# Optimization experiments

Measured on AMD Instinct MI355X. Metric: run time of the kernel, lower is better.

## Reference

```python
import jax, jax.numpy as jnp
import numpy as np

N_NODES = 500_000
N_EDGES = 8_000_000
N_GRAPHS = 512
N_FEATURES = 128
HIDDEN = 128
N_FILT = 8
OUT_DIM = 64
BN_EPS = 1e-5


def setup_inputs() -> dict:
    key = jax.random.key(0)
    ks = jax.random.split(key, 16)
    rn = lambda k, shape, s=0.05: jax.random.normal(k, shape, jnp.float32) * s
    return {
        "x": jax.random.normal(ks[0], (N_NODES, N_FEATURES), jnp.float32),
        "W1": rn(ks[1], (N_FEATURES, HIDDEN)),
        "b1": jnp.zeros((HIDDEN,), jnp.float32),
        "W2": rn(ks[2], (HIDDEN, N_FILT)),
        "b2": jnp.zeros((N_FILT,), jnp.float32),
        "W0": rn(ks[3], (2 * N_FILT, OUT_DIM)),
        "b0": jnp.zeros((OUT_DIM,), jnp.float32),
        "g1W": rn(ks[4], (OUT_DIM, OUT_DIM)),
        "g1b": jnp.zeros((OUT_DIM,), jnp.float32),
        "l1W": rn(ks[5], (OUT_DIM, OUT_DIM)),
        "g2W": rn(ks[6], (OUT_DIM, N_FEATURES)),
        "g2b": jnp.zeros((N_FEATURES,), jnp.float32),
        "l2W": rn(ks[7], (OUT_DIM, N_FEATURES)),
        "bn_gamma": jnp.ones((N_FEATURES,), jnp.float32),
        "bn_beta": jnp.zeros((N_FEATURES,), jnp.float32),
        "edge_index": jax.random.randint(ks[8], (2, N_EDGES), 0, N_NODES),
        "batch": jnp.sort(jax.random.randint(ks[9], (N_NODES,), 0, N_GRAPHS)),
        "death_edge_idx": jax.random.randint(ks[10], (N_NODES,), 0, N_EDGES),
    }


def _deepset(x, batch, GW, Gb, LW):
    # scatter-mean over graphs, Linear (no bias), gather-broadcast subtract
    sums = jax.ops.segment_sum(x, batch, num_segments=N_GRAPHS)  # [G, d]
    cnt = jax.ops.segment_sum(jnp.ones((x.shape[0], 1), x.dtype), batch,
                              num_segments=N_GRAPHS)             # [G, 1]
    xm = (sums / jnp.maximum(cnt, 1.0)) @ LW                      # Lambda
    return x @ GW + Gb - xm[batch]                                # Gamma - gather


def reference(x, W1, b1, W2, b2, W0, b0, g1W, g1b, l1W, g2W, g2b, l2W,
              bn_gamma, bn_beta, edge_index, batch, death_edge_idx):
    # filtrations MLP: [N, F] -> [N, n_filtrations]
    filtered_v = jax.nn.relu(x @ W1 + b1) @ W2 + b2
    # edge filtration = max of endpoint values (gather + max), [E, n_filtrations]
    filtered_e = jnp.maximum(filtered_v[edge_index[0]], filtered_v[edge_index[1]])
    # persistence pairs (lower-star 0-dim generators): birth = vertex value,
    # death = paired edge value; layout [N, n_filt, 2] -> [N, 2*n_filt]
    births = filtered_v
    deaths = filtered_e[death_edge_idx]
    x0 = jnp.stack([births, deaths], axis=-1).reshape(x.shape[0], 2 * N_FILT)
    # set_fn: Linear -> ReLU -> DeepSet -> ReLU -> DeepSet
    x0 = jax.nn.relu(x0 @ W0 + b0)
    x0 = jax.nn.relu(_deepset(x0, batch, g1W, g1b, l1W))
    x0 = _deepset(x0, batch, g2W, g2b, l2W)
    # residual: x + BatchNorm1d(relu(x0)) with batch statistics
    h = jax.nn.relu(x0)
    mu = h.mean(axis=0)
    var = h.var(axis=0)
    hn = (h - mu) * jax.lax.rsqrt(var + BN_EPS)
    return x + hn * bn_gamma + bn_beta
```

## Files before the change

kernel.cpp:

```cpp
#include <hip/hip_runtime.h>
#include <hip/hip_bf16.h>

#define NNODES 500000
#define NEDGES 8000000
#define NGRAPHS 512
#define NFEAT 128
#define NHID 128
#define NFILT 8
#define ODIM 64
#define BN_EPS 1e-5f
#define NBLK2 3907
#define NBLK3 7813
#define NBLK4 977

typedef __attribute__((ext_vector_type(8))) short bf16x8;
typedef __attribute__((ext_vector_type(4))) float f32x4;
#define MFMA16(a, b, c) __builtin_amdgcn_mfma_f32_16x16x32_bf16(a, b, c, 0, 0, 0)

__device__ inline ushort f2bs(float f) {
  union { __hip_bfloat16 h; ushort u; } cv;
  cv.h = __float2bfloat16(f);
  return cv.u;
}

__global__ void k_pack(const float* __restrict__ g1W, const float* __restrict__ g2W,
                       const float* __restrict__ W1, const int* __restrict__ batch,
                       ushort* __restrict__ pW1, ushort* __restrict__ pW2,
                       ushort* __restrict__ pW0, int* __restrict__ cnt) {
  int idx = blockIdx.x * 256 + threadIdx.x;
  if (idx < 4096) {
    int j = idx & 7, l = (idx >> 3) & 63, kb = (idx >> 9) & 1, ncb = idx >> 10;
    int k = kb * 32 + (l >> 4) * 8 + j, c = ncb * 16 + (l & 15);
    pW1[idx] = f2bs(g1W[k * 64 + c]);
  }
  if (idx < 8192) {
    int j = idx & 7, l = (idx >> 3) & 63, kb = (idx >> 9) & 1, ncb = idx >> 10;
    int k = kb * 32 + (l >> 4) * 8 + j, c = ncb * 16 + (l & 15);
    pW2[idx] = f2bs(g2W[k * 128 + c]);
  }
  if (idx < 16384) {
    int j = idx & 7, l = (idx >> 3) & 63, kb = (idx >> 9) & 3, ncb = idx >> 11;
    int k = kb * 32 + (l >> 4) * 8 + j, c = ncb * 16 + (l & 15);
    pW0[idx] = f2bs(W1[k * 128 + c]);
  }
  if (idx < NGRAPHS) {
    int g = idx;
    int lo0 = 0, hi0 = NNODES;
    while (lo0 < hi0) { int mid = (lo0 + hi0) >> 1; if (batch[mid] < g) lo0 = mid + 1; else hi0 = mid; }
    int lo1 = lo0, hi1 = NNODES;
    while (lo1 < hi1) { int mid = (lo1 + hi1) >> 1; if (batch[mid] < g + 1) lo1 = mid + 1; else hi1 = mid; }
    cnt[g] = lo1 - lo0;
  }
}

__global__ __launch_bounds__(256) void k_filt(
    const float* __restrict__ x, const ushort* __restrict__ pW0,
    const float* __restrict__ b1, const float* __restrict__ W2,
    const float* __restrict__ b2, float* __restrict__ fv) {
  __shared__ float w2s[128 * 12];
  const int t = threadIdx.x;
  for (int i = t; i < 1024; i += 256) {
    int c = i >> 3, f = i & 7;
    w2s[c * 12 + f] = W2[i];
  }
  __syncthreads();
  const int wv = t >> 6, l = t & 63;
  const int lr = l & 15, lg = l >> 4;
  const int n0 = blockIdx.x * 128 + wv * 32;
  if (n0 >= NNODES) return;

  union { uint4 u; bf16x8 b; } bf[2][4];
#pragma unroll
  for (int mt = 0; mt < 2; ++mt)
#pragma unroll
    for (int kb = 0; kb < 4; ++kb) {
      const float* src = &x[(size_t)(n0 + mt * 16 + lr) * 128 + kb * 32 + lg * 8];
      float v[8];
      *(float4*)&v[0] = *(const float4*)src;
      *(float4*)&v[4] = *(const float4*)(src + 4);
      ushort s[8];
#pragma unroll
      for (int e = 0; e < 8; ++e) s[e] = f2bs(v[e]);
      bf[mt][kb].u = *(uint4*)s;
    }

  float pf0[8], pf1[8];
#pragma unroll
  for (int f = 0; f < 8; ++f) { pf0[f] = 0.f; pf1[f] = 0.f; }

#pragma unroll
  for (int ncb = 0; ncb < 8; ++ncb) {
    union { uint4 u; bf16x8 b; } af[4];
#pragma unroll
    for (int kb = 0; kb < 4; ++kb)
      af[kb].u = *(const uint4*)&pW0[((ncb * 4 + kb) * 64 + l) * 8];
    f32x4 a0 = (f32x4){0.f, 0.f, 0.f, 0.f};
    f32x4 a1 = (f32x4){0.f, 0.f, 0.f, 0.f};
#pragma unroll
    for (int kb = 0; kb < 4; ++kb) {
      a0 = MFMA16(af[kb].b, bf[0][kb].b, a0);
      a1 = MFMA16(af[kb].b, bf[1][kb].b, a1);
    }
    float bbv[4];
    *(float4*)bbv = *(const float4*)&b1[ncb * 16 + lg * 4];
#pragma unroll
    for (int r = 0; r < 4; ++r) {
      const int c = ncb * 16 + lg * 4 + r;
      float h0 = fmaxf(a0[r] + bbv[r], 0.f);
      float h1 = fmaxf(a1[r] + bbv[r], 0.f);
      float w20[4], w21[4];
      *(float4*)w20 = *(const float4*)&w2s[c * 12];
      *(float4*)w21 = *(const float4*)&w2s[c * 12 + 4];
#pragma unroll
      for (int f = 0; f < 4; ++f) {
        pf0[f]     = fmaf(h0, w20[f], pf0[f]);
        pf0[f + 4] = fmaf(h0, w21[f], pf0[f + 4]);
        pf1[f]     = fmaf(h1, w20[f], pf1[f]);
        pf1[f + 4] = fmaf(h1, w21[f], pf1[f + 4]);
      }
    }
  }
#pragma unroll
  for (int f = 0; f < 8; ++f) {
    pf0[f] += __shfl_xor(pf0[f], 16); pf0[f] += __shfl_xor(pf0[f], 32);
    pf1[f] += __shfl_xor(pf1[f], 16); pf1[f] += __shfl_xor(pf1[f], 32);
  }
  if (lg == 0) {
    float o0[8], o1[8];
#pragma unroll
    for (int f = 0; f < 8; ++f) {
      float bb = b2[f];
      o0[f] = pf0[f] + bb;
      o1[f] = pf1[f] + bb;
    }
    *(float4*)&fv[(size_t)(n0 + lr) * 8]          = *(float4*)&o0[0];
    *(float4*)&fv[(size_t)(n0 + lr) * 8 + 4]      = *(float4*)&o0[4];
    *(float4*)&fv[(size_t)(n0 + 16 + lr) * 8]     = *(float4*)&o1[0];
    *(float4*)&fv[(size_t)(n0 + 16 + lr) * 8 + 4] = *(float4*)&o1[4];
  }
}

__global__ __launch_bounds__(256) void k_pairs(
    const float* __restrict__ fv, const int* __restrict__ edge_index,
    const int* __restrict__ didx, const int* __restrict__ batch,
    const float* __restrict__ W0, const float* __restrict__ b0,
    ushort* __restrict__ y, float* __restrict__ sums1) {
  __shared__ float w0s[16 * 64];
  __shared__ float b0s[64];
  __shared__ float ps[4][64];
  __shared__ int pg[4];
  const int t = threadIdx.x;
  for (int i = t; i < 1024; i += 256) w0s[i] = W0[i];
  if (t < 64) b0s[t] = b0[t];
  __syncthreads();

  const int wv = t >> 6, j = t & 63;
  const int n0 = blockIdx.x * 128 + wv * 32;

  int de = 0, gg = -1, uu = 0, vvx = 0;
  if (j < 32) {
    int nn = n0 + j;
    if (nn < NNODES) { de = didx[nn]; gg = batch[nn]; }
  }
  if (j < 32 && gg >= 0) { uu = edge_index[de]; vvx = edge_index[NEDGES + de]; }

  const float bb = b0s[j];
  float acc0 = 0.f, acc1 = 0.f;
  int g_first = -1, g_second = -1;

#pragma unroll 4
  for (int i = 0; i < 32; ++i) {
    int g = __shfl(gg, i);
    if (g >= 0) {
      int u = __shfl(uu, i);
      int v = __shfl(vvx, i);
      int n = n0 + i;
      float nb[8], ub[8], vb[8];
      *(float4*)&nb[0] = *(const float4*)&fv[(size_t)n * 8];
      *(float4*)&nb[4] = *(const float4*)&fv[(size_t)n * 8 + 4];
      *(float4*)&ub[0] = *(const float4*)&fv[(size_t)u * 8];
      *(float4*)&ub[4] = *(const float4*)&fv[(size_t)u * 8 + 4];
      *(float4*)&vb[0] = *(const float4*)&fv[(size_t)v * 8];
      *(float4*)&vb[4] = *(const float4*)&fv[(size_t)v * 8 + 4];
      float a = bb;
#pragma unroll
      for (int f = 0; f < 8; ++f) {
        a = fmaf(nb[f], w0s[(2 * f) * 64 + j], a);
        a = fmaf(fmaxf(ub[f], vb[f]), w0s[(2 * f + 1) * 64 + j], a);
      }
      a = fmaxf(a, 0.f);
      y[(size_t)n * 64 + j] = f2bs(a);
      if (g_first < 0) g_first = g;
      if (g == g_first) acc0 += a;
      else { g_second = g; acc1 += a; }
    }
  }
  if (g_second >= 0) atomicAdd(&sums1[g_second * 64 + j], acc1);
  ps[wv][j] = acc0;
  if (j == 0) pg[wv] = g_first;
  __syncthreads();

  if (t < 64) {
    const int bg = pg[0];
    float s = 0.f;
#pragma unroll
    for (int w = 0; w < 4; ++w) {
      const int gv = pg[w];
      if (gv < 0) continue;
      if (gv == bg) s += ps[w][t];
      else atomicAdd(&sums1[gv * 64 + t], ps[w][t]);
    }
    if (bg >= 0) atomicAdd(&sums1[bg * 64 + t], s);
  }
}

template <int D>
__global__ void k_meanlin(const float* __restrict__ sums,
                          const int* __restrict__ cnt,
                          const float* __restrict__ LW,
                          float* __restrict__ xm) {
  __shared__ float m[64];
  const int g = blockIdx.x, t = threadIdx.x;
  const float c = fmaxf((float)cnt[g], 1.f);
  if (t < 64) m[t] = sums[g * 64 + t] / c;
  __syncthreads();
  float a = 0.f;
#pragma unroll
  for (int k = 0; k < 64; ++k) a = fmaf(m[k], LW[k * D + t], a);
  xm[g * D + t] = a;
}

__global__ __launch_bounds__(256) void k_ds1(
    const ushort* __restrict__ ybf, const int* __restrict__ batch,
    const ushort* __restrict__ pW1, const float* __restrict__ g1b,
    const float* __restrict__ xm1, ushort* __restrict__ y2,
    float* __restrict__ sums2) {
  __shared__ float ps[4][64];
  __shared__ int pg[4];
  const int t = threadIdx.x, wv = t >> 6, l = t & 63;
  const int lr = l & 15, lg = l >> 4, c0 = lg * 4;
  const int nbase = blockIdx.x * 512;

  union { uint4 u; bf16x8 b; } af[4][2];
#pragma unroll
  for (int ncb = 0; ncb < 4; ++ncb)
#pragma unroll
    for (int kb = 0; kb < 2; ++kb)
      af[ncb][kb].u = *(const uint4*)&pW1[((ncb * 2 + kb) * 64 + l) * 8];

  for (int tile = 0; tile < 4; ++tile) {
    const int n0 = nbase + tile * 128 + wv * 32;
    if (n0 < NNODES) {
      union { uint4 u; bf16x8 b; } bf[2][2];
#pragma unroll
      for (int mt = 0; mt < 2; ++mt)
#pragma unroll
        for (int kb = 0; kb < 2; ++kb)
          bf[mt][kb].u = *(const uint4*)&ybf[(size_t)(n0 + mt * 16 + lr) * 64 + kb * 32 + lg * 8];

      f32x4 acc[2][4];
#pragma unroll
      for (int mt = 0; mt < 2; ++mt)
#pragma unroll
        for (int ncb = 0; ncb < 4; ++ncb) {
          acc[mt][ncb] = (f32x4){0.f, 0.f, 0.f, 0.f};
          acc[mt][ncb] = MFMA16(af[ncb][0].b, bf[mt][0].b, acc[mt][ncb]);
          acc[mt][ncb] = MFMA16(af[ncb][1].b, bf[mt][1].b, acc[mt][ncb]);
        }

      const int g0 = batch[n0 + lr], g1 = batch[n0 + 16 + lr];
      const int g_first = __shfl(g0, 0);

      float wsum[4][4];
#pragma unroll
      for (int ncb = 0; ncb < 4; ++ncb)
#pragma unroll
        for (int r = 0; r < 4; ++r) wsum[ncb][r] = 0.f;

#pragma unroll
      for (int mt = 0; mt < 2; ++mt) {
        const int n = n0 + mt * 16 + lr;
        const int g = mt ? g1 : g0;
        const bool prim = (g == g_first);
#pragma unroll
        for (int ncb = 0; ncb < 4; ++ncb) {
          const int c = ncb * 16 + c0;
          float xmv[4], bbv[4];
          *(float4*)xmv = *(const float4*)&xm1[g * 64 + c];
          *(float4*)bbv = *(const float4*)&g1b[c];
          ushort st[4];
#pragma unroll
          for (int r = 0; r < 4; ++r) {
            float v = fmaxf(acc[mt][ncb][r] + bbv[r] - xmv[r], 0.f);
            st[r] = f2bs(v);
            if (prim) wsum[ncb][r] += v;
            else atomicAdd(&sums2[g * 64 + c + r], v);
          }
          *(ushort4*)&y2[(size_t)n * 64 + c] = *(ushort4*)st;
        }
      }
#pragma unroll
      for (int ncb = 0; ncb < 4; ++ncb)
#pragma unroll
        for (int r = 0; r < 4; ++r) {
          float w = wsum[ncb][r];
          w += __shfl_xor(w, 1); w += __shfl_xor(w, 2);
          w += __shfl_xor(w, 4); w += __shfl_xor(w, 8);
          if (lr == 0) ps[wv][ncb * 16 + c0 + r] = w;
        }
      if (l == 0) pg[wv] = g_first;
    } else {
      ps[wv][l] = 0.f;
      if (l == 0) pg[wv] = -1;
    }
    __syncthreads();

    if (t < 64) {
      const int bg = pg[0];
      float s = 0.f;
#pragma unroll
      for (int w = 0; w < 4; ++w) {
        const int gv = pg[w];
        if (gv < 0) continue;
        if (gv == bg) s += ps[w][t];
        else atomicAdd(&sums2[gv * 64 + t], ps[w][t]);
      }
      if (bg >= 0) atomicAdd(&sums2[bg * 64 + t], s);
    }
    __syncthreads();
  }
}

__global__ __launch_bounds__(256) void k_ds2a(
    const ushort* __restrict__ y2, const int* __restrict__ batch,
    const ushort* __restrict__ pW2, const float* __restrict__ g2b,
    const float* __restrict__ xm2,
    float* __restrict__ pmu, float* __restrict__ psq) {
  __shared__ float ps[4][128], pq[4][128];
  const int t = threadIdx.x, wv = t >> 6, l = t & 63;
  const int lr = l & 15, lg = l >> 4, c0 = lg * 4;
  const int nbase = blockIdx.x * 512;

  float sw[8][4], sq[8][4];
#pragma unroll
  for (int ncb = 0; ncb < 8; ++ncb)
#pragma unroll
    for (int r = 0; r < 4; ++r) { sw[ncb][r] = 0.f; sq[ncb][r] = 0.f; }

  for (int tile = 0; tile < 4; ++tile) {
    const int n0 = nbase + tile * 128 + wv * 32;
    if (n0 >= NNODES) continue;

    union { uint4 u; bf16x8 b; } bf[2][2];
#pragma unroll
    for (int mt = 0; mt < 2; ++mt)
#pragma unroll
      for (int kb = 0; kb < 2; ++kb)
        bf[mt][kb].u = *(const uint4*)&y2[(size_t)(n0 + mt * 16 + lr) * 64 + kb * 32 + lg * 8];

    const int g0 = batch[n0 + lr], g1 = batch[n0 + 16 + lr];

#pragma unroll
    for (int ncb = 0; ncb < 8; ++ncb) {
      union { uint4 u; bf16x8 b; } af0, af1;
      af0.u = *(const uint4*)&pW2[((ncb * 2 + 0) * 64 + l) * 8];
      af1.u = *(const uint4*)&pW2[((ncb * 2 + 1) * 64 + l) * 8];
      f32x4 a0 = (f32x4){0.f, 0.f, 0.f, 0.f}, a1 = (f32x4){0.f, 0.f, 0.f, 0.f};
      a0 = MFMA16(af0.b, bf[0][0].b, a0); a0 = MFMA16(af1.b, bf[0][1].b, a0);
      a1 = MFMA16(af0.b, bf[1][0].b, a1); a1 = MFMA16(af1.b, bf[1][1].b, a1);

      const int c = ncb * 16 + c0;
      float xm0[4], xm1v[4], bbv[4];
      *(float4*)xm0 = *(const float4*)&xm2[g0 * 128 + c];
      *(float4*)xm1v = *(const float4*)&xm2[g1 * 128 + c];
      *(float4*)bbv = *(const float4*)&g2b[c];
#pragma unroll
      for (int r = 0; r < 4; ++r) {
        float v0 = fmaxf(a0[r] + bbv[r] - xm0[r], 0.f);
        float v1 = fmaxf(a1[r] + bbv[r] - xm1v[r], 0.f);
        sw[ncb][r] += v0 + v1;
        sq[ncb][r] = fmaf(v0, v0, fmaf(v1, v1, sq[ncb][r]));
      }
    }
  }

#pragma unroll
  for (int ncb = 0; ncb < 8; ++ncb)
#pragma unroll
    for (int r = 0; r < 4; ++r) {
      float wr = sw[ncb][r], qr = sq[ncb][r];
      wr += __shfl_xor(wr, 1); wr += __shfl_xor(wr, 2);
      wr += __shfl_xor(wr, 4); wr += __shfl_xor(wr, 8);
      qr += __shfl_xor(qr, 1); qr += __shfl_xor(qr, 2);
      qr += __shfl_xor(qr, 4); qr += __shfl_xor(qr, 8);
      if (lr == 0) { ps[wv][ncb * 16 + c0 + r] = wr; pq[wv][ncb * 16 + c0 + r] = qr; }
    }
  __syncthreads();
  if (t < 128) {
    pmu[(size_t)blockIdx.x * 128 + t] = ps[0][t] + ps[1][t] + ps[2][t] + ps[3][t];
    psq[(size_t)blockIdx.x * 128 + t] = pq[0][t] + pq[1][t] + pq[2][t] + pq[3][t];
  }
}

__global__ void k_red(const float* __restrict__ pmu, const float* __restrict__ psq,
                      float* __restrict__ musum, float* __restrict__ sqsum) {
  const int f = threadIdx.x & 127;
  const bool mu = threadIdx.x < 128;
  const float* src = mu ? pmu : psq;
  float s = 0.f;
  for (int b = blockIdx.x; b < NBLK4; b += 32) s += src[(size_t)b * 128 + f];
  atomicAdd(mu ? &musum[f] : &sqsum[f], s);
}

__global__ __launch_bounds__(256) void k_bn(
    const ushort* __restrict__ y2, const int* __restrict__ batch,
    const ushort* __restrict__ pW2, const float* __restrict__ g2b,
    const float* __restrict__ xm2, const float* __restrict__ x,
    const float* __restrict__ musum, const float* __restrict__ sqsum,
    const float* __restrict__ gamma, const float* __restrict__ beta,
    float* __restrict__ out) {
  __shared__ float vs[64 * 132];
  __shared__ float smu[128], ssc[128], sbe[128];
  const int t = threadIdx.x, wv = t >> 6, l = t & 63;
  const int lr = l & 15, lg = l >> 4, c0 = lg * 4;
  if (t < 128) {
    const float invN = 1.f / (float)NNODES;
    float m = musum[t] * invN;
    float v = sqsum[t] * invN - m * m;
    smu[t] = m;
    ssc[t] = rsqrtf(v + BN_EPS) * gamma[t];
    sbe[t] = beta[t];
  }
  const int nblk = blockIdx.x * 64;
  const int n0 = nblk + wv * 16;

  if (n0 < NNODES) {
    union { uint4 u; bf16x8 b; } bf[2];
#pragma unroll
    for (int kb = 0; kb < 2; ++kb)
      bf[kb].u = *(const uint4*)&y2[(size_t)(n0 + lr) * 64 + kb * 32 + lg * 8];

    const int g0 = batch[n0 + lr];
    const int row0 = wv * 16 + lr;

#pragma unroll
    for (int ncb = 0; ncb < 8; ++ncb) {
      union { uint4 u; bf16x8 b; } af0, af1;
      af0.u = *(const uint4*)&pW2[((ncb * 2 + 0) * 64 + l) * 8];
      af1.u = *(const uint4*)&pW2[((ncb * 2 + 1) * 64 + l) * 8];
      f32x4 a0 = (f32x4){0.f, 0.f, 0.f, 0.f};
      a0 = MFMA16(af0.b, bf[0].b, a0);
      a0 = MFMA16(af1.b, bf[1].b, a0);

      const int c = ncb * 16 + c0;
      float bbv[4], xm0[4], hvv[4];
      *(float4*)bbv = *(const float4*)&g2b[c];
      *(float4*)xm0 = *(const float4*)&xm2[g0 * 128 + c];
#pragma unroll
      for (int r = 0; r < 4; ++r)
        hvv[r] = fmaxf(a0[r] + bbv[r] - xm0[r], 0.f);
      *(float4*)&vs[row0 * 132 + c] = *(float4*)hvv;
    }
  }
  __syncthreads();

  const int rmax = NNODES - nblk;
  for (int i = t; i < 2048; i += 256) {
    const int row = i >> 5, c4 = (i & 31) * 4;
    if (row >= rmax) break;
    const int n = nblk + row;
    float hv[4], muv[4], scv[4], bev[4], xv[4], o[4];
    *(float4*)hv = *(const float4*)&vs[row * 132 + c4];
    *(float4*)muv = *(const float4*)&smu[c4];
    *(float4*)scv = *(const float4*)&ssc[c4];
    *(float4*)bev = *(const float4*)&sbe[c4];
    *(float4*)xv = *(const float4*)&x[(size_t)n * 128 + c4];
#pragma unroll
    for (int r = 0; r < 4; ++r)
      o[r] = xv[r] + (hv[r] - muv[r]) * scv[r] + bev[r];
    *(float4*)&out[(size_t)n * 128 + c4] = *(float4*)o;
  }
}

extern "C" void kernel_launch(void* const* d_in, const int* in_sizes, int n_in,
                              void* d_out, int out_size, void* d_ws,
                              size_t ws_size, hipStream_t stream) {
  const float* x     = (const float*)d_in[0];
  const float* W1    = (const float*)d_in[1];
  const float* b1    = (const float*)d_in[2];
  const float* W2    = (const float*)d_in[3];
  const float* b2    = (const float*)d_in[4];
  const float* W0    = (const float*)d_in[5];
  const float* b0    = (const float*)d_in[6];
  const float* g1W   = (const float*)d_in[7];
  const float* g1b   = (const float*)d_in[8];
  const float* l1W   = (const float*)d_in[9];
  const float* g2W   = (const float*)d_in[10];
  const float* g2b   = (const float*)d_in[11];
  const float* l2W   = (const float*)d_in[12];
  const float* gamma = (const float*)d_in[13];
  const float* beta  = (const float*)d_in[14];
  const int* edge_index = (const int*)d_in[15];
  const int* batch      = (const int*)d_in[16];
  const int* didx       = (const int*)d_in[17];
  float* out = (float*)d_out;

  char* ws = (char*)d_ws;
  float*  fv    = (float*) (ws + 0);
  float*  pmu   = (float*) (ws + 0);
  float*  psq   = (float*) (ws + 2000384);
  ushort* ybf   = (ushort*)(ws + 16000000);
  ushort* y2    = (ushort*)(ws + 80000000);
  float*  sums1 = (float*) (ws + 144000000);
  float*  sums2 = (float*) (ws + 144131072);
  float*  musum = (float*) (ws + 144262144);
  float*  sqsum = (float*) (ws + 144262656);
  int*    cnt   = (int*)   (ws + 144263168);
  float*  xm1   = (float*) (ws + 144265216);
  float*  xm2   = (float*) (ws + 144396288);
  ushort* pW1   = (ushort*)(ws + 144658432);
  ushort* pW2   = (ushort*)(ws + 144666624);
  ushort* pW0   = (ushort*)(ws + 144683008);

  hipMemsetAsync(ws + 144000000, 0, 263168, stream);

  k_pack<<<64, 256, 0, stream>>>(g1W, g2W, W1, batch, pW1, pW2, pW0, cnt);
  k_filt<<<NBLK2, 256, 0, stream>>>(x, pW0, b1, W2, b2, fv);
  k_pairs<<<NBLK2, 256, 0, stream>>>(fv, edge_index, didx, batch, W0, b0, ybf, sums1);
  k_meanlin<64><<<NGRAPHS, 64, 0, stream>>>(sums1, cnt, l1W, xm1);
  k_ds1<<<NBLK4, 256, 0, stream>>>(ybf, batch, pW1, g1b, xm1, y2, sums2);
  k_meanlin<128><<<NGRAPHS, 128, 0, stream>>>(sums2, cnt, l2W, xm2);
  k_ds2a<<<NBLK4, 256, 0, stream>>>(y2, batch, pW2, g2b, xm2, pmu, psq);
  k_red<<<32, 256, 0, stream>>>(pmu, psq, musum, sqsum);
  k_bn<<<NBLK3, 256, 0, stream>>>(y2, batch, pW2, g2b, xm2, x, musum, sqsum,
                                  gamma, beta, out);
}
```

Measured before the change: 541.3 us.

## Store filtration values as bf16 and compute pair linear layer with MFMA

Filtration values are now written as bf16, which halves the fv buffer and the bytes moved by the random gathers in the pairs kernel. The 16x64 pair linear layer moves from per-lane scalar FMAs to a bf16 MFMA, using a zero-padded packed W0 built in the pack kernel. Each pairs block now covers four 128-node tiles, and per-graph sums are reduced with shuffles before the atomics. In exchange, births and deaths lose precision to bf16, and nodes outside the first graph of a wave fall back to per-element atomics.

```diff
diff --git a/kernel.cpp b/kernel.cpp
--- a/kernel.cpp
+++ b/kernel.cpp
@@ -24,9 +24,11 @@
 }
 
 __global__ void k_pack(const float* __restrict__ g1W, const float* __restrict__ g2W,
-                       const float* __restrict__ W1, const int* __restrict__ batch,
+                       const float* __restrict__ W1, const float* __restrict__ W0,
+                       const int* __restrict__ batch,
                        ushort* __restrict__ pW1, ushort* __restrict__ pW2,
-                       ushort* __restrict__ pW0, int* __restrict__ cnt) {
+                       ushort* __restrict__ pW0, ushort* __restrict__ pW0p,
+                       int* __restrict__ cnt) {
   int idx = blockIdx.x * 256 + threadIdx.x;
   if (idx < 4096) {
     int j = idx & 7, l = (idx >> 3) & 63, kb = (idx >> 9) & 1, ncb = idx >> 10;
@@ -42,6 +44,11 @@
     int j = idx & 7, l = (idx >> 3) & 63, kb = (idx >> 9) & 3, ncb = idx >> 11;
     int k = kb * 32 + (l >> 4) * 8 + j, c = ncb * 16 + (l & 15);
     pW0[idx] = f2bs(W1[k * 128 + c]);
+  }
+  if (idx < 4096) {
+    int j = idx & 7, l = (idx >> 3) & 63, ncb = idx >> 9;
+    int k = (l >> 4) * 8 + j, c = ncb * 16 + (l & 15);
+    pW0p[idx] = (k < 16) ? f2bs(W0[k * 64 + c]) : (ushort)0;
   }
   if (idx < NGRAPHS) {
     int g = idx;
@@ -56,7 +63,7 @@
 __global__ __launch_bounds__(256) void k_filt(
     const float* __restrict__ x, const ushort* __restrict__ pW0,
     const float* __restrict__ b1, const float* __restrict__ W2,
-    const float* __restrict__ b2, float* __restrict__ fv) {
+    const float* __restrict__ b2, ushort* __restrict__ fv16) {
   __shared__ float w2s[128 * 12];
   const int t = threadIdx.x;
   for (int i = t; i < 1024; i += 256) {
@@ -126,91 +133,132 @@
     pf1[f] += __shfl_xor(pf1[f], 16); pf1[f] += __shfl_xor(pf1[f], 32);
   }
   if (lg == 0) {
-    float o0[8], o1[8];
+    ushort s0[8], s1[8];
 #pragma unroll
     for (int f = 0; f < 8; ++f) {
       float bb = b2[f];
-      o0[f] = pf0[f] + bb;
-      o1[f] = pf1[f] + bb;
-    }
-    *(float4*)&fv[(size_t)(n0 + lr) * 8]          = *(float4*)&o0[0];
-    *(float4*)&fv[(size_t)(n0 + lr) * 8 + 4]      = *(float4*)&o0[4];
-    *(float4*)&fv[(size_t)(n0 + 16 + lr) * 8]     = *(float4*)&o1[0];
-    *(float4*)&fv[(size_t)(n0 + 16 + lr) * 8 + 4] = *(float4*)&o1[4];
+      s0[f] = f2bs(pf0[f] + bb);
+      s1[f] = f2bs(pf1[f] + bb);
+    }
+    *(uint4*)&fv16[(size_t)(n0 + lr) * 8]      = *(uint4*)s0;
+    *(uint4*)&fv16[(size_t)(n0 + 16 + lr) * 8] = *(uint4*)s1;
   }
 }
 
 __global__ __launch_bounds__(256) void k_pairs(
-    const float* __restrict__ fv, const int* __restrict__ edge_index,
+    const ushort* __restrict__ fv16, const int* __restrict__ edge_index,
     const int* __restrict__ didx, const int* __restrict__ batch,
-    const float* __restrict__ W0, const float* __restrict__ b0,
+    const ushort* __restrict__ pW0p, const float* __restrict__ b0,
     ushort* __restrict__ y, float* __restrict__ sums1) {
-  __shared__ float w0s[16 * 64];
-  __shared__ float b0s[64];
   __shared__ float ps[4][64];
   __shared__ int pg[4];
-  const int t = threadIdx.x;
-  for (int i = t; i < 1024; i += 256) w0s[i] = W0[i];
-  if (t < 64) b0s[t] = b0[t];
-  __syncthreads();
-
-  const int wv = t >> 6, j = t & 63;
-  const int n0 = blockIdx.x * 128 + wv * 32;
-
-  int de = 0, gg = -1, uu = 0, vvx = 0;
-  if (j < 32) {
-    int nn = n0 + j;
-    if (nn < NNODES) { de = didx[nn]; gg = batch[nn]; }
-  }
-  if (j < 32 && gg >= 0) { uu = edge_index[de]; vvx = edge_index[NEDGES + de]; }
-
-  const float bb = b0s[j];
-  float acc0 = 0.f, acc1 = 0.f;
-  int g_first = -1, g_second = -1;
-
-#pragma unroll 4
-  for (int i = 0; i < 32; ++i) {
-    int g = __shfl(gg, i);
-    if (g >= 0) {
-      int u = __shfl(uu, i);
-      int v = __shfl(vvx, i);
-      int n = n0 + i;
-      float nb[8], ub[8], vb[8];
-      *(float4*)&nb[0] = *(const float4*)&fv[(size_t)n * 8];
-      *(float4*)&nb[4] = *(const float4*)&fv[(size_t)n * 8 + 4];
-      *(float4*)&ub[0] = *(const float4*)&fv[(size_t)u * 8];
-      *(float4*)&ub[4] = *(const float4*)&fv[(size_t)u * 8 + 4];
-      *(float4*)&vb[0] = *(const float4*)&fv[(size_t)v * 8];
-      *(float4*)&vb[4] = *(const float4*)&fv[(size_t)v * 8 + 4];
-      float a = bb;
-#pragma unroll
-      for (int f = 0; f < 8; ++f) {
-        a = fmaf(nb[f], w0s[(2 * f) * 64 + j], a);
-        a = fmaf(fmaxf(ub[f], vb[f]), w0s[(2 * f + 1) * 64 + j], a);
-      }
-      a = fmaxf(a, 0.f);
-      y[(size_t)n * 64 + j] = f2bs(a);
-      if (g_first < 0) g_first = g;
-      if (g == g_first) acc0 += a;
-      else { g_second = g; acc1 += a; }
-    }
-  }
-  if (g_second >= 0) atomicAdd(&sums1[g_second * 64 + j], acc1);
-  ps[wv][j] = acc0;
-  if (j == 0) pg[wv] = g_first;
-  __syncthreads();
-
-  if (t < 64) {
-    const int bg = pg[0];
-    float s = 0.f;
-#pragma unroll
-    for (int w = 0; w < 4; ++w) {
-      const int gv = pg[w];
-      if (gv < 0) continue;
-      if (gv == bg) s += ps[w][t];
-      else atomicAdd(&sums1[gv * 64 + t], ps[w][t]);
-    }
-    if (bg >= 0) atomicAdd(&sums1[bg * 64 + t], s);
+  const int t = threadIdx.x, wv = t >> 6, l = t & 63;
+  const int lr = l & 15, lg = l >> 4, c0 = lg * 4;
+  const int nbase = blockIdx.x * 512;
+
+  union { uint4 u; bf16x8 b; } af[4];
+#pragma unroll
+  for (int ncb = 0; ncb < 4; ++ncb)
+    af[ncb].u = *(const uint4*)&pW0p[(ncb * 64 + l) * 8];
+
+  for (int tile = 0; tile < 4; ++tile) {
+    const int n0 = nbase + tile * 128 + wv * 32;
+    if (n0 < NNODES) {
+      union { uint4 u; bf16x8 b; } bf[2];
+      int gN[2];
+#pragma unroll
+      for (int mt = 0; mt < 2; ++mt) {
+        const int n = n0 + mt * 16 + lr;
+        gN[mt] = batch[n];
+        bf[mt].u = make_uint4(0u, 0u, 0u, 0u);
+        if (lg < 2) {
+          const int de = didx[n];
+          const int u = edge_index[de];
+          const int v = edge_index[NEDGES + de];
+          ushort4 bb = *(const ushort4*)&fv16[(size_t)n * 8 + lg * 4];
+          ushort4 ub = *(const ushort4*)&fv16[(size_t)u * 8 + lg * 4];
+          ushort4 vb = *(const ushort4*)&fv16[(size_t)v * 8 + lg * 4];
+          const ushort* bp = (const ushort*)&bb;
+          const ushort* up = (const ushort*)&ub;
+          const ushort* vp = (const ushort*)&vb;
+          ushort s[8];
+#pragma unroll
+          for (int j = 0; j < 4; ++j) {
+            s[2 * j] = bp[j];
+            float uf = __uint_as_float((unsigned)up[j] << 16);
+            float vf = __uint_as_float((unsigned)vp[j] << 16);
+            s[2 * j + 1] = (uf > vf) ? up[j] : vp[j];
+          }
+          bf[mt].u = *(uint4*)s;
+        }
+      }
+
+      f32x4 acc[2][4];
+#pragma unroll
+      for (int mt = 0; mt < 2; ++mt)
+#pragma unroll
+        for (int ncb = 0; ncb < 4; ++ncb) {
+          acc[mt][ncb] = (f32x4){0.f, 0.f, 0.f, 0.f};
+          acc[mt][ncb] = MFMA16(af[ncb].b, bf[mt].b, acc[mt][ncb]);
+        }
+
+      const int g_first = __shfl(gN[0], 0);
+      float wsum[4][4];
+#pragma unroll
+      for (int ncb = 0; ncb < 4; ++ncb)
+#pragma unroll
+        for (int r = 0; r < 4; ++r) wsum[ncb][r] = 0.f;
+
+#pragma unroll
+      for (int mt = 0; mt < 2; ++mt) {
+        const int n = n0 + mt * 16 + lr;
+        const int g = gN[mt];
+        const bool prim = (g == g_first);
+#pragma unroll
+        for (int ncb = 0; ncb < 4; ++ncb) {
+          const int c = ncb * 16 + c0;
+          float bbv[4];
+          *(float4*)bbv = *(const float4*)&b0[c];
+          ushort st[4];
+#pragma unroll
+          for (int r = 0; r < 4; ++r) {
+            float v = fmaxf(acc[mt][ncb][r] + bbv[r], 0.f);
+            st[r] = f2bs(v);
+            if (prim) wsum[ncb][r] += v;
+            else atomicAdd(&sums1[g * 64 + c + r], v);
+          }
+          *(ushort4*)&y[(size_t)n * 64 + c] = *(ushort4*)st;
+        }
+      }
+#pragma unroll
+      for (int ncb = 0; ncb < 4; ++ncb)
+#pragma unroll
+        for (int r = 0; r < 4; ++r) {
+          float w = wsum[ncb][r];
+          w += __shfl_xor(w, 1); w += __shfl_xor(w, 2);
+          w += __shfl_xor(w, 4); w += __shfl_xor(w, 8);
+          if (lr == 0) ps[wv][ncb * 16 + c0 + r] = w;
+        }
+      if (l == 0) pg[wv] = g_first;
+    } else {
+      ps[wv][l] = 0.f;
+      if (l == 0) pg[wv] = -1;
+    }
+    __syncthreads();
+
+    if (t < 64) {
+      const int bg = pg[0];
+      float s = 0.f;
+#pragma unroll
+      for (int w = 0; w < 4; ++w) {
+        const int gv = pg[w];
+        if (gv < 0) continue;
+        if (gv == bg) s += ps[w][t];
+        else atomicAdd(&sums1[gv * 64 + t], ps[w][t]);
+      }
+      if (bg >= 0) atomicAdd(&sums1[bg * 64 + t], s);
+    }
+    __syncthreads();
   }
 }
 
@@ -506,7 +554,7 @@
   float* out = (float*)d_out;
 
   char* ws = (char*)d_ws;
-  float*  fv    = (float*) (ws + 0);
+  ushort* fv16  = (ushort*)(ws + 0);
   float*  pmu   = (float*) (ws + 0);
   float*  psq   = (float*) (ws + 2000384);
   ushort* ybf   = (ushort*)(ws + 16000000);
@@ -521,12 +569,13 @@
   ushort* pW1   = (ushort*)(ws + 144658432);
   ushort* pW2   = (ushort*)(ws + 144666624);
   ushort* pW0   = (ushort*)(ws + 144683008);
+  ushort* pW0p  = (ushort*)(ws + 144715776);
 
   hipMemsetAsync(ws + 144000000, 0, 263168, stream);
 
-  k_pack<<<64, 256, 0, stream>>>(g1W, g2W, W1, batch, pW1, pW2, pW0, cnt);
-  k_filt<<<NBLK2, 256, 0, stream>>>(x, pW0, b1, W2, b2, fv);
-  k_pairs<<<NBLK2, 256, 0, stream>>>(fv, edge_index, didx, batch, W0, b0, ybf, sums1);
+  k_pack<<<64, 256, 0, stream>>>(g1W, g2W, W1, W0, batch, pW1, pW2, pW0, pW0p, cnt);
+  k_filt<<<NBLK2, 256, 0, stream>>>(x, pW0, b1, W2, b2, fv16);
+  k_pairs<<<NBLK4, 256, 0, stream>>>(fv16, edge_index, didx, batch, pW0p, b0, ybf, sums1);
   k_meanlin<64><<<NGRAPHS, 64, 0, stream>>>(sums1, cnt, l1W, xm1);
   k_ds1<<<NBLK4, 256, 0, stream>>>(ybf, batch, pW1, g1b, xm1, y2, sums2);
   k_meanlin<128><<<NGRAPHS, 128, 0, stream>>>(sums2, cnt, l2W, xm2);
```

Result: faster. 523.4 us (-3.3%).
